# Optimization experiments

Measured on AMD Instinct MI355X. Metric: run time of the kernel, lower is better.

## Reference

```python
import jax, jax.numpy as jnp
import numpy as np

D_MODEL = 1024
N_HEAD = 16
D_HEAD = D_MODEL // N_HEAD
EXP = 4
B, T = 2, 2048
EPS = 1e-5

def setup_inputs() -> dict:
    key = jax.random.key(0)
    ks = jax.random.split(key, 16)
    s = 0.02
    return {
        "x": jax.random.normal(ks[0], (B, T, D_MODEL), jnp.float32),
        "ln1_w": jnp.ones((D_MODEL,), jnp.float32),
        "ln1_b": jnp.zeros((D_MODEL,), jnp.float32),
        "attn_w": jax.random.normal(ks[1], (D_MODEL, 3 * D_MODEL), jnp.float32) * s,
        "attn_b": jnp.zeros((3 * D_MODEL,), jnp.float32),
        "proj_w": jax.random.normal(ks[2], (D_MODEL, D_MODEL), jnp.float32) * s,
        "proj_b": jnp.zeros((D_MODEL,), jnp.float32),
        "ln2_w": jnp.ones((D_MODEL,), jnp.float32),
        "ln2_b": jnp.zeros((D_MODEL,), jnp.float32),
        "fc_w": jax.random.normal(ks[3], (D_MODEL, EXP * D_MODEL), jnp.float32) * s,
        "fc_b": jnp.zeros((EXP * D_MODEL,), jnp.float32),
        "fc2_w": jax.random.normal(ks[4], (EXP * D_MODEL, D_MODEL), jnp.float32) * s,
        "fc2_b": jnp.zeros((D_MODEL,), jnp.float32),
    }

def _layernorm(x, w, b):
    mu = jnp.mean(x, axis=-1, keepdims=True)
    var = jnp.mean(jnp.square(x - mu), axis=-1, keepdims=True)
    return (x - mu) * jax.lax.rsqrt(var + EPS) * w + b

def _attn(x, attn_w, attn_b, proj_w, proj_b):
    Bx, Tx, C = x.shape
    qkv = x @ attn_w + attn_b  # [B,T,3C]
    q, k, v = jnp.split(qkv, 3, axis=-1)
    # [B, H, T, Dh]
    q = q.reshape(Bx, Tx, N_HEAD, D_HEAD).transpose(0, 2, 1, 3)
    k = k.reshape(Bx, Tx, N_HEAD, D_HEAD).transpose(0, 2, 1, 3)
    v = v.reshape(Bx, Tx, N_HEAD, D_HEAD).transpose(0, 2, 1, 3)
    att = jnp.einsum('bhqd,bhkd->bhqk', q, k) * (1.0 / np.sqrt(D_HEAD))
    causal = jnp.tril(jnp.ones((Tx, Tx), bool))
    att = jnp.where(causal, att, -jnp.inf)
    att = jax.nn.softmax(att, axis=-1)
    y = jnp.einsum('bhqk,bhkd->bhqd', att, v)
    y = y.transpose(0, 2, 1, 3).reshape(Bx, Tx, C)
    return y @ proj_w + proj_b

def reference(x, ln1_w, ln1_b, attn_w, attn_b, proj_w, proj_b,
              ln2_w, ln2_b, fc_w, fc_b, fc2_w, fc2_b):
    x = x + _attn(_layernorm(x, ln1_w, ln1_b), attn_w, attn_b, proj_w, proj_b)
    h = _layernorm(x, ln2_w, ln2_b)
    h = jax.nn.gelu(h @ fc_w + fc_b, approximate=False)  # exact GELU (torch nn.GELU default)
    x = x + (h @ fc2_w + fc2_b)
    return x
```

## Files before the change

kernel.cpp:

```cpp
#include <hip/hip_runtime.h>
#include <hip/hip_bf16.h>
#include <math.h>


#define D_MODEL 1024
#define N_HEAD  16
#define D_HEAD  64
#define SEQ_T   2048
#define BATCH   2
#define NROWS   (BATCH * SEQ_T)
#define C3      (3 * D_MODEL)
#define D_FF    (4 * D_MODEL)

typedef __bf16 bf16x8 __attribute__((ext_vector_type(8)));
typedef __bf16 bf16x4t __attribute__((ext_vector_type(4)));
typedef short  s16x4  __attribute__((ext_vector_type(4)));
typedef float  f32x4  __attribute__((ext_vector_type(4)));

#define WAIT_VM0() asm volatile("s_waitcnt vmcnt(0)" ::: "memory")
#define WAIT_VM2() asm volatile("s_waitcnt vmcnt(2)" ::: "memory")
#define WAIT_VM4() asm volatile("s_waitcnt vmcnt(4)" ::: "memory")

__device__ __forceinline__ f32x4 mfma16_bf16(s16x4 a, s16x4 b, f32x4 c)
{
#if __has_builtin(__builtin_amdgcn_mfma_f32_16x16x16_bf16)
    return __builtin_amdgcn_mfma_f32_16x16x16_bf16(
        __builtin_bit_cast(bf16x4t, a), __builtin_bit_cast(bf16x4t, b), c, 0, 0, 0);
#else
    return __builtin_amdgcn_mfma_f32_16x16x16bf16_1k(a, b, c, 0, 0, 0);
#endif
}

__global__ __launch_bounds__(256) void ln_kernel(
    const float* __restrict__ in, const float* __restrict__ w,
    const float* __restrict__ b, __hip_bfloat16* __restrict__ out, int D)
{
    const int row = blockIdx.x;
    const int tid = threadIdx.x;
    const float* x = in + (size_t)row * 1024;

    const float4 v = *(const float4*)(x + tid * 4);
    float s  = v.x + v.y + v.z + v.w;
    float s2 = v.x * v.x + v.y * v.y + v.z * v.z + v.w * v.w;

    __shared__ float rs[256], rs2[256];
    rs[tid] = s; rs2[tid] = s2;
    __syncthreads();
    for (int off = 128; off > 0; off >>= 1) {
        if (tid < off) { rs[tid] += rs[tid + off]; rs2[tid] += rs2[tid + off]; }
        __syncthreads();
    }
    const float mu   = rs[0] * (1.0f / 1024.0f);
    const float var  = rs2[0] * (1.0f / 1024.0f) - mu * mu;
    const float rstd = rsqrtf(var + 1e-5f);

    const float4 w4 = *(const float4*)(w + tid * 4);
    const float4 b4 = *(const float4*)(b + tid * 4);
    float o[4] = {(v.x - mu) * rstd * w4.x + b4.x,
                  (v.y - mu) * rstd * w4.y + b4.y,
                  (v.z - mu) * rstd * w4.z + b4.z,
                  (v.w - mu) * rstd * w4.w + b4.w};
    ushort4 pk;
    { __hip_bfloat16 e0 = __float2bfloat16(o[0]); pk.x = *(unsigned short*)&e0;
      __hip_bfloat16 e1 = __float2bfloat16(o[1]); pk.y = *(unsigned short*)&e1;
      __hip_bfloat16 e2 = __float2bfloat16(o[2]); pk.z = *(unsigned short*)&e2;
      __hip_bfloat16 e3 = __float2bfloat16(o[3]); pk.w = *(unsigned short*)&e3; }
    *(ushort4*)(out + (size_t)row * 1024 + tid * 4) = pk;
}

__global__ __launch_bounds__(256) void prep_kernel(
    const float* __restrict__ attn_w, const float* __restrict__ proj_w,
    const float* __restrict__ fc_w,   const float* __restrict__ fc2_w,
    __hip_bfloat16* __restrict__ attn_wt, __hip_bfloat16* __restrict__ proj_wt,
    __hip_bfloat16* __restrict__ fc_wt,   __hip_bfloat16* __restrict__ fc2_wt,
    const float* __restrict__ x, const float* __restrict__ ln1_w,
    const float* __restrict__ ln1_b, __hip_bfloat16* __restrict__ ln_out)
{
    __shared__ float smem[32 * 33];
    int tb = blockIdx.x;
    const int tid = threadIdx.x;

    if (tb >= 12288) {
        const int row = tb - 12288;
        const float* xr = x + (size_t)row * 1024;
        const float4 v = *(const float4*)(xr + tid * 4);
        float s  = v.x + v.y + v.z + v.w;
        float s2 = v.x * v.x + v.y * v.y + v.z * v.z + v.w * v.w;
        float* rs  = smem;
        float* rs2 = smem + 256;
        rs[tid] = s; rs2[tid] = s2;
        __syncthreads();
        for (int off = 128; off > 0; off >>= 1) {
            if (tid < off) { rs[tid] += rs[tid + off]; rs2[tid] += rs2[tid + off]; }
            __syncthreads();
        }
        const float mu   = rs[0] * (1.0f / 1024.0f);
        const float var  = rs2[0] * (1.0f / 1024.0f) - mu * mu;
        const float rstd = rsqrtf(var + 1e-5f);
        const float4 w4 = *(const float4*)(ln1_w + tid * 4);
        const float4 b4 = *(const float4*)(ln1_b + tid * 4);
        float o[4] = {(v.x - mu) * rstd * w4.x + b4.x,
                      (v.y - mu) * rstd * w4.y + b4.y,
                      (v.z - mu) * rstd * w4.z + b4.z,
                      (v.w - mu) * rstd * w4.w + b4.w};
        ushort4 pk;
        { __hip_bfloat16 e0 = __float2bfloat16(o[0]); pk.x = *(unsigned short*)&e0;
          __hip_bfloat16 e1 = __float2bfloat16(o[1]); pk.y = *(unsigned short*)&e1;
          __hip_bfloat16 e2 = __float2bfloat16(o[2]); pk.z = *(unsigned short*)&e2;
          __hip_bfloat16 e3 = __float2bfloat16(o[3]); pk.w = *(unsigned short*)&e3; }
        *(ushort4*)(ln_out + (size_t)row * 1024 + tid * 4) = pk;
        return;
    }

    float (*t)[33] = (float(*)[33])smem;
    const float* W; __hip_bfloat16* Wt; int K, N;
    if (tb < 3072)      { W = attn_w; Wt = attn_wt; K = D_MODEL; N = C3; }
    else if (tb < 4096) { tb -= 3072; W = proj_w; Wt = proj_wt; K = D_MODEL; N = D_MODEL; }
    else if (tb < 8192) { tb -= 4096; W = fc_w;   Wt = fc_wt;   K = D_MODEL; N = D_FF; }
    else                { tb -= 8192; W = fc2_w;  Wt = fc2_wt;  K = D_FF;    N = D_MODEL; }
    const int ntx = N >> 5;
    const int k0 = (tb / ntx) * 32;
    const int n0 = (tb % ntx) * 32;

    const int row = tid >> 3;
    const int c4  = (tid & 7) * 4;

    const float4 v = *(const float4*)&W[(size_t)(k0 + row) * N + n0 + c4];
    t[row][c4 + 0] = v.x; t[row][c4 + 1] = v.y;
    t[row][c4 + 2] = v.z; t[row][c4 + 3] = v.w;
    __syncthreads();

    ushort4 pk;
    { __hip_bfloat16 e0 = __float2bfloat16(t[c4 + 0][row]); pk.x = *(unsigned short*)&e0;
      __hip_bfloat16 e1 = __float2bfloat16(t[c4 + 1][row]); pk.y = *(unsigned short*)&e1;
      __hip_bfloat16 e2 = __float2bfloat16(t[c4 + 2][row]); pk.z = *(unsigned short*)&e2;
      __hip_bfloat16 e3 = __float2bfloat16(t[c4 + 3][row]); pk.w = *(unsigned short*)&e3; }
    *(ushort4*)&Wt[(size_t)(n0 + row) * K + k0 + c4] = pk;
}

__device__ __forceinline__ void async16(const __hip_bfloat16* g, __hip_bfloat16* l)
{
    __builtin_amdgcn_global_load_lds(
        (const __attribute__((address_space(1))) void*)g,
        (__attribute__((address_space(3))) void*)l, 16, 0, 0);
}

__device__ __forceinline__ float gelu_fast(float v)
{
    const float t = v * (0.7978845608f + 0.0356774081f * v * v);
    return v / (1.0f + exp2f(-2.885390082f * t));
}

__device__ __forceinline__ void swz_xcd(int& bx, int& by)
{
    const int nbx = gridDim.x;
    const int nwg = nbx * gridDim.y;
    int lin = blockIdx.y * nbx + blockIdx.x;
    const int per = nwg >> 3;
    lin = (lin & 7) * per + (lin >> 3);
    bx = lin % nbx;
    by = lin / nbx;
}


__device__ __forceinline__ void gemm8p_core(
    const __hip_bfloat16* __restrict__ A,
    const __hip_bfloat16* __restrict__ Bt,
    int K, int row0, int col0, f32x4 (&acc)[8][4],
    __hip_bfloat16 (*Asl)[4][64 * 64], __hip_bfloat16 (*Bsl)[2][128 * 64])
{
    const int tid  = threadIdx.x;
    const int wv   = tid >> 6;
    const int lane = tid & 63;
    const int ln15 = lane & 15;
    const int lq   = lane >> 4;
    const int wr   = wv >> 2;
    const int wc   = wv & 3;

    const int srow = tid >> 3;
    const int sg   = ((tid & 7) ^ ((tid >> 3) & 7)) * 8;
    const __hip_bfloat16* Ab = A  + (size_t)(row0 + srow) * K + sg;
    const __hip_bfloat16* Bb = Bt + (size_t)(col0 + srow) * K + sg;
    const int nt = K >> 6;

#pragma unroll
    for (int mi = 0; mi < 8; ++mi)
#pragma unroll
        for (int ni = 0; ni < 4; ++ni) acc[mi][ni] = (f32x4){0.f, 0.f, 0.f, 0.f};

    auto stA = [&](int t, int buf, int b) {
        async16(Ab + (size_t)(b * 64) * K + t * 64, &Asl[buf][b][0] + tid * 8);
    };
    auto stB = [&](int t, int buf, int h) {
        async16(Bb + (size_t)(h * 128) * K + t * 64, &Bsl[buf][h][0] + tid * 8);
        async16(Bb + (size_t)(h * 128 + 64) * K + t * 64,
                &Bsl[buf][h][0] + 4096 + tid * 8);
    };

    const int rg0 = (lq ^ (ln15 & 7)) * 8;
    const int rg1 = ((4 | lq) ^ (ln15 & 7)) * 8;
    auto ldA = [&](int buf, int mi, int kk) -> bf16x8 {
        return *(const bf16x8*)&Asl[buf][wr * 2 + (mi >> 2)]
            [((mi & 3) * 16 + ln15) * 64 + (kk ? rg1 : rg0)];
    };
    auto ldB = [&](int buf, int ni, int kk) -> bf16x8 {
        return *(const bf16x8*)&Bsl[buf][wc >> 1]
            [((wc & 1) * 64 + ni * 16 + ln15) * 64 + (kk ? rg1 : rg0)];
    };

    stB(0, 0, 0); stB(0, 0, 1);
    stA(0, 0, 0); stA(0, 0, 2); stA(0, 0, 1); stA(0, 0, 3);
    WAIT_VM0();
    __builtin_amdgcn_s_barrier();

    for (int t = 0; t < nt; ++t) {
        const int pp = t & 1, op = pp ^ 1;
        const int tc = (t + 1 < nt) ? t + 1 : nt - 1;
        bf16x8 af[2][2], bfr[4][2];

#pragma unroll
        for (int m = 0; m < 2; ++m) { af[m][0] = ldA(pp, m, 0); af[m][1] = ldA(pp, m, 1); }
#pragma unroll
        for (int ni = 0; ni < 4; ++ni) { bfr[ni][0] = ldB(pp, ni, 0); bfr[ni][1] = ldB(pp, ni, 1); }
        stB(tc, op, 0);
        __builtin_amdgcn_s_barrier();
        __builtin_amdgcn_s_setprio(1);
#pragma unroll
        for (int kk = 0; kk < 2; ++kk)
#pragma unroll
            for (int m = 0; m < 2; ++m)
#pragma unroll
                for (int ni = 0; ni < 4; ++ni)
                    acc[m][ni] = __builtin_amdgcn_mfma_f32_16x16x32_bf16(
                        af[m][kk], bfr[ni][kk], acc[m][ni], 0, 0, 0);
        __builtin_amdgcn_s_setprio(0);
        __builtin_amdgcn_s_barrier();

#pragma unroll
        for (int m = 0; m < 2; ++m) { af[m][0] = ldA(pp, 2 + m, 0); af[m][1] = ldA(pp, 2 + m, 1); }
        stB(tc, op, 1);
        WAIT_VM4();
        __builtin_amdgcn_s_barrier();
        __builtin_amdgcn_s_setprio(1);
#pragma unroll
        for (int kk = 0; kk < 2; ++kk)
#pragma unroll
            for (int m = 0; m < 2; ++m)
#pragma unroll
                for (int ni = 0; ni < 4; ++ni)
                    acc[2 + m][ni] = __builtin_amdgcn_mfma_f32_16x16x32_bf16(
                        af[m][kk], bfr[ni][kk], acc[2 + m][ni], 0, 0, 0);
        __builtin_amdgcn_s_setprio(0);
        __builtin_amdgcn_s_barrier();

#pragma unroll
        for (int m = 0; m < 2; ++m) { af[m][0] = ldA(pp, 4 + m, 0); af[m][1] = ldA(pp, 4 + m, 1); }
        stA(tc, op, 0); stA(tc, op, 2);
        __builtin_amdgcn_s_barrier();
        __builtin_amdgcn_s_setprio(1);
#pragma unroll
        for (int kk = 0; kk < 2; ++kk)
#pragma unroll
            for (int m = 0; m < 2; ++m)
#pragma unroll
                for (int ni = 0; ni < 4; ++ni)
                    acc[4 + m][ni] = __builtin_amdgcn_mfma_f32_16x16x32_bf16(
                        af[m][kk], bfr[ni][kk], acc[4 + m][ni], 0, 0, 0);
        __builtin_amdgcn_s_setprio(0);
        __builtin_amdgcn_s_barrier();

#pragma unroll
        for (int m = 0; m < 2; ++m) { af[m][0] = ldA(pp, 6 + m, 0); af[m][1] = ldA(pp, 6 + m, 1); }
        stA(tc, op, 1); stA(tc, op, 3);
        WAIT_VM2();
        __builtin_amdgcn_s_barrier();
        __builtin_amdgcn_s_setprio(1);
#pragma unroll
        for (int kk = 0; kk < 2; ++kk)
#pragma unroll
            for (int m = 0; m < 2; ++m)
#pragma unroll
                for (int ni = 0; ni < 4; ++ni)
                    acc[6 + m][ni] = __builtin_amdgcn_mfma_f32_16x16x32_bf16(
                        af[m][kk], bfr[ni][kk], acc[6 + m][ni], 0, 0, 0);
        __builtin_amdgcn_s_setprio(0);
        __builtin_amdgcn_s_barrier();
    }
}

__global__ __launch_bounds__(512, 1) void gemm8p_kernel(
    const __hip_bfloat16* __restrict__ A,
    const __hip_bfloat16* __restrict__ Bt,
    const float* __restrict__ bias,
    __hip_bfloat16* __restrict__ Cout,
    int M, int N, int K, int act)
{
    __shared__ __align__(16) __hip_bfloat16 Asl[2][4][64 * 64];
    __shared__ __align__(16) __hip_bfloat16 Bsl[2][2][128 * 64];

    int bx, by;
    swz_xcd(bx, by);
    const int row0 = by * 256;
    const int col0 = bx * 256;

    f32x4 acc[8][4];
    gemm8p_core(A, Bt, K, row0, col0, acc, Asl, Bsl);

    const int tid  = threadIdx.x;
    const int wv   = tid >> 6;
    const int lane = tid & 63;
    const int ln15 = lane & 15;
    const int lq   = lane >> 4;
    const int mbase = (wv >> 2) * 128;
    const int nbase = (wv & 3) * 64;

#pragma unroll
    for (int mi = 0; mi < 8; ++mi) {
#pragma unroll
        for (int ni = 0; ni < 4; ++ni) {
            const int gc = col0 + nbase + ni * 16 + ln15;
            const float bv = bias[gc];
#pragma unroll
            for (int r = 0; r < 4; ++r) {
                const int gr = row0 + mbase + mi * 16 + lq * 4 + r;
                float v = acc[mi][ni][r] + bv;
                if (act == 1) v = gelu_fast(v);
                Cout[(size_t)gr * N + gc] = __float2bfloat16(v);
            }
        }
    }
}

__global__ __launch_bounds__(512, 1) void qkv8p_kernel(
    const __hip_bfloat16* __restrict__ A,
    const __hip_bfloat16* __restrict__ Bt,
    const float* __restrict__ bias,
    __hip_bfloat16* __restrict__ Qb,
    __hip_bfloat16* __restrict__ Kb,
    __hip_bfloat16* __restrict__ Vtb)
{
    __shared__ __align__(16) __hip_bfloat16 Asl[2][4][64 * 64];
    __shared__ __align__(16) __hip_bfloat16 Bsl[2][2][128 * 64];

    int bx, by;
    swz_xcd(bx, by);
    const int row0 = by * 256;
    const int col0 = bx * 256;

    f32x4 acc[8][4];
    gemm8p_core(A, Bt, D_MODEL, row0, col0, acc, Asl, Bsl);

    const int tid  = threadIdx.x;
    const int wv   = tid >> 6;
    const int lane = tid & 63;
    const int ln15 = lane & 15;
    const int lq   = lane >> 4;
    const int mbase = (wv >> 2) * 128;
    const int nbase = (wv & 3) * 64;

#pragma unroll
    for (int mi = 0; mi < 8; ++mi) {
        const int gr0 = row0 + mbase + mi * 16 + lq * 4;
        const int bb  = gr0 >> 11;
        const int q0  = gr0 & 2047;
#pragma unroll
        for (int ni = 0; ni < 4; ++ni) {
            const int gc  = col0 + nbase + ni * 16 + ln15;
            const float bv = bias[gc];
            const int sec = gc >> 10;
            const int hd  = (gc & 1023) >> 6;
            const int d   = gc & 63;
            if (sec == 2) {
                unsigned short u[4];
#pragma unroll
                for (int r = 0; r < 4; ++r) {
                    __hip_bfloat16 e = __float2bfloat16(acc[mi][ni][r] + bv);
                    u[r] = *(unsigned short*)&e;
                }
                uint2 pk;
                pk.x = (unsigned int)u[0] | ((unsigned int)u[1] << 16);
                pk.y = (unsigned int)u[2] | ((unsigned int)u[3] << 16);
                *(uint2*)(Vtb + ((size_t)((bb * N_HEAD + hd) * D_HEAD + d)) * SEQ_T + q0) = pk;
            } else {
                __hip_bfloat16* dst = (sec == 0 ? Qb : Kb)
                    + ((size_t)((bb * N_HEAD + hd) * SEQ_T + q0)) * D_HEAD + d;
#pragma unroll
                for (int r = 0; r < 4; ++r)
                    dst[(size_t)r * D_HEAD] = __float2bfloat16(acc[mi][ni][r] + bv);
            }
        }
    }
}

__device__ __forceinline__ void stage_db2w(
    const __hip_bfloat16* __restrict__ Ab, const __hip_bfloat16* __restrict__ Bb,
    int K, int kt, __hip_bfloat16* __restrict__ as,
    __hip_bfloat16* __restrict__ bs, int tid)
{
    const int k0 = kt * 64;
#pragma unroll
    for (int s = 0; s < 2; ++s) {
        async16(Ab + k0 + s * 32, as + s * 64 * 32 + tid * 8);
#pragma unroll
        for (int i = 0; i < 2; ++i)
            async16(Bb + (size_t)(i * 64) * K + k0 + s * 32,
                    bs + s * 128 * 32 + i * 64 * 32 + tid * 8);
    }
}

__device__ __forceinline__ void gemm_db2w(
    const __hip_bfloat16* __restrict__ A,
    const __hip_bfloat16* __restrict__ Bt,
    int K, int row0, int col0, f32x4 (&acc)[2][4])
{
    __shared__ __align__(16) __hip_bfloat16 Asl[2][2 * 64 * 32];
    __shared__ __align__(16) __hip_bfloat16 Bsl[2][2 * 128 * 32];

    const int tid  = threadIdx.x;
    const int wv   = tid >> 6;
    const int lane = tid & 63;
    const int ln15 = lane & 15;
    const int lq   = lane >> 4;
    const int mbase = (wv >> 1) * 32;
    const int nbase = (wv & 1) * 64;
    const int rcol = (lq ^ ((ln15 >> 1) & 3)) * 8;
    const int ssw  = ((tid & 3) ^ ((tid >> 3) & 3)) * 8;
    const __hip_bfloat16* Ab = A  + (size_t)(row0 + (tid >> 2)) * K + ssw;
    const __hip_bfloat16* Bb = Bt + (size_t)(col0 + (tid >> 2)) * K + ssw;
    const int nt = K >> 6;

#pragma unroll
    for (int mi = 0; mi < 2; ++mi)
#pragma unroll
        for (int ni = 0; ni < 4; ++ni) acc[mi][ni] = (f32x4){0.f, 0.f, 0.f, 0.f};

    stage_db2w(Ab, Bb, K, 0, &Asl[0][0], &Bsl[0][0], tid);
    WAIT_VM0();
    __builtin_amdgcn_s_barrier();

    for (int t = 0; t < nt; ++t) {
        const int p   = t & 1;
        const int tcl = (t + 1 < nt) ? t + 1 : nt - 1;
        bf16x8 af[2][2], bfr[2][4];

#pragma unroll
        for (int s = 0; s < 2; ++s) {
#pragma unroll
            for (int mi = 0; mi < 2; ++mi)
                af[s][mi] = *(const bf16x8*)
                    &Asl[p][s * 64 * 32 + (mbase + mi * 16 + ln15) * 32 + rcol];
#pragma unroll
            for (int ni = 0; ni < 4; ++ni)
                bfr[s][ni] = *(const bf16x8*)
                    &Bsl[p][s * 128 * 32 + (nbase + ni * 16 + ln15) * 32 + rcol];
        }

        stage_db2w(Ab, Bb, K, tcl, &Asl[p ^ 1][0], &Bsl[p ^ 1][0], tid);

        __builtin_amdgcn_s_setprio(1);
#pragma unroll
        for (int s = 0; s < 2; ++s)
#pragma unroll
            for (int mi = 0; mi < 2; ++mi)
#pragma unroll
                for (int ni = 0; ni < 4; ++ni)
                    acc[mi][ni] = __builtin_amdgcn_mfma_f32_16x16x32_bf16(
                        af[s][mi], bfr[s][ni], acc[mi][ni], 0, 0, 0);
        __builtin_amdgcn_s_setprio(0);

        WAIT_VM0();
        __builtin_amdgcn_s_barrier();
    }
}

__global__ __launch_bounds__(256, 3) void gemm64_kernel(
    const __hip_bfloat16* __restrict__ A,
    const __hip_bfloat16* __restrict__ Bt,
    const float* __restrict__ bias,
    const float* __restrict__ residual,
    void* __restrict__ Cout,
    int M, int N, int K, int act, int outBf16)
{
    int bx, by;
    swz_xcd(bx, by);
    const int row0 = by * 64;
    const int col0 = bx * 128;

    f32x4 acc[2][4];
    gemm_db2w(A, Bt, K, row0, col0, acc);

    const int tid  = threadIdx.x;
    const int wv   = tid >> 6;
    const int lane = tid & 63;
    const int ln15 = lane & 15;
    const int lq   = lane >> 4;
    const int mbase = (wv >> 1) * 32;
    const int nbase = (wv & 1) * 64;

#pragma unroll
    for (int mi = 0; mi < 2; ++mi) {
#pragma unroll
        for (int ni = 0; ni < 4; ++ni) {
            const int gc = col0 + nbase + ni * 16 + ln15;
            const float bv = bias[gc];
#pragma unroll
            for (int r = 0; r < 4; ++r) {
                const int gr = row0 + mbase + mi * 16 + lq * 4 + r;
                float v = acc[mi][ni][r] + bv;
                if (act == 1) v = gelu_fast(v);
                if (residual) v += residual[(size_t)gr * N + gc];
                if (outBf16)
                    ((__hip_bfloat16*)Cout)[(size_t)gr * N + gc] = __float2bfloat16(v);
                else
                    ((float*)Cout)[(size_t)gr * N + gc] = v;
            }
        }
    }
}

#define ATQ 64
#define ATK 128
#define NQT (SEQ_T / ATQ)
#define VP2 136

__global__ __launch_bounds__(256) void mfma_attn_kernel(
    const __hip_bfloat16* __restrict__ Qb,
    const __hip_bfloat16* __restrict__ Kb,
    const __hip_bfloat16* __restrict__ Vtb,
    __hip_bfloat16* __restrict__ y)
{
    __shared__ __align__(16) __hip_bfloat16 Ks[2 * ATK * 32];
    __shared__ __align__(16) __hip_bfloat16 Vts[D_HEAD * VP2];

    const int flat = (blockIdx.z * gridDim.y + blockIdx.y) * gridDim.x + blockIdx.x;
    const int xcd  = flat & 7;
    const int slot = flat >> 3;
    const int pair = slot & 15;
    const int hb   = slot >> 4;
    const int h    = xcd + 8 * (hb & 1);
    const int b    = hb >> 1;

    const int tid  = threadIdx.x;
    const int wv   = tid >> 6;
    const int lane = tid & 63;
    const int ln15 = lane & 15;
    const int lq   = lane >> 4;

    const __hip_bfloat16* Qh = Qb  + (size_t)(b * N_HEAD + h) * SEQ_T * D_HEAD;
    const __hip_bfloat16* Kh = Kb  + (size_t)(b * N_HEAD + h) * SEQ_T * D_HEAD;
    const __hip_bfloat16* Vh = Vtb + (size_t)(b * N_HEAD + h) * D_HEAD * SEQ_T;
    const size_t bT = (size_t)b * SEQ_T;

    const float CEXP = 0.18033688011f;
    const float DTHR = 8.0f / CEXP;

    bf16x8 kreg[4], vreg[4];
    const int kr = tid >> 3, kg = tid & 7;
    const int vr = tid >> 4, vc = tid & 15;
    const int khalf = kg >> 2;
    const int kpos  = (kg & 3) ^ ((kr >> 1) & 3);

    auto issue = [&](int kb) {
#pragma unroll
        for (int i = 0; i < 4; ++i)
            kreg[i] = *(const bf16x8*)(Kh + (size_t)(kb + kr + i * 32) * D_HEAD + kg * 8);
#pragma unroll
        for (int i = 0; i < 4; ++i)
            vreg[i] = *(const bf16x8*)(Vh + (size_t)(vr + i * 16) * SEQ_T + kb + vc * 8);
    };
    auto commit = [&]() {
#pragma unroll
        for (int i = 0; i < 4; ++i) {
            const int r = kr + i * 32;
            *(bf16x8*)&Ks[khalf * (ATK * 32) + r * 32 + kpos * 8] = kreg[i];
        }
#pragma unroll
        for (int i = 0; i < 4; ++i) {
            const int r = vr + i * 16;
            *(bf16x8*)&Vts[r * VP2 + vc * 8] = vreg[i];
        }
    };

    const int rcol = (lq ^ ((ln15 >> 1) & 3)) * 8;

#pragma unroll 1
    for (int half = 0; half < 2; ++half) {
        const int qt    = half == 0 ? pair : (NQT - 1 - pair);
        const int qbase = qt * ATQ;
        const int ntk   = (qt >> 1) + 1;
        const int qg    = qbase + wv * 16 + ln15;

        bf16x8 qf[2];
#pragma unroll
        for (int kc = 0; kc < 2; ++kc)
            qf[kc] = *(const bf16x8*)(Qh + (size_t)(qbase + wv * 16 + ln15) * D_HEAD
                                      + kc * 32 + lq * 8);

        f32x4 Oacc[4];
#pragma unroll
        for (int dn = 0; dn < 4; ++dn) Oacc[dn] = (f32x4){0.f, 0.f, 0.f, 0.f};
        float m_run = -INFINITY, l_run = 0.f;

        issue(0);

        for (int t = 0; t < ntk; ++t) {
            const int kb = t * ATK;
            commit();
            __syncthreads();
            if (t + 1 < ntk) issue((t + 1) * ATK);

            f32x4 st[8];
#pragma unroll
            for (int jf = 0; jf < 8; ++jf) st[jf] = (f32x4){0.f, 0.f, 0.f, 0.f};
            __builtin_amdgcn_s_setprio(1);
#pragma unroll
            for (int jf = 0; jf < 8; ++jf) {
                const int rw = jf * 16 + ln15;
                const bf16x8 kf0 = *(const bf16x8*)&Ks[rw * 32 + rcol];
                const bf16x8 kf1 = *(const bf16x8*)&Ks[ATK * 32 + rw * 32 + rcol];
                st[jf] = __builtin_amdgcn_mfma_f32_16x16x32_bf16(kf0, qf[0], st[jf], 0, 0, 0);
                st[jf] = __builtin_amdgcn_mfma_f32_16x16x32_bf16(kf1, qf[1], st[jf], 0, 0, 0);
            }
            __builtin_amdgcn_s_setprio(0);

            if (t == ntk - 1) {
#pragma unroll
                for (int jf = 0; jf < 8; ++jf)
#pragma unroll
                    for (int r = 0; r < 4; ++r)
                        if ((kb + jf * 16 + lq * 4 + r) > qg) st[jf][r] = -INFINITY;
            }

            float tmax = st[0][0];
#pragma unroll
            for (int jf = 0; jf < 8; ++jf)
#pragma unroll
                for (int r = 0; r < 4; ++r) tmax = fmaxf(tmax, st[jf][r]);
            tmax = fmaxf(tmax, __shfl_xor(tmax, 16));
            tmax = fmaxf(tmax, __shfl_xor(tmax, 32));

            if (!__all(tmax <= m_run + DTHR)) {
                const float mnew  = fmaxf(m_run, tmax);
                const float alpha = exp2f((m_run - mnew) * CEXP);
                l_run *= alpha;
                m_run = mnew;
                float a4[4];
#pragma unroll
                for (int r = 0; r < 4; ++r) a4[r] = __shfl(alpha, lq * 4 + r);
#pragma unroll
                for (int dn = 0; dn < 4; ++dn)
#pragma unroll
                    for (int r = 0; r < 4; ++r) Oacc[dn][r] *= a4[r];
            }
            const float mc = m_run * CEXP;
            float psum = 0.f;
#pragma unroll
            for (int jf = 0; jf < 8; ++jf)
#pragma unroll
                for (int r = 0; r < 4; ++r) {
                    const float p = exp2f(fmaf(st[jf][r], CEXP, -mc));
                    st[jf][r] = p;
                    psum += p;
                }
            psum += __shfl_xor(psum, 16);
            psum += __shfl_xor(psum, 32);
            l_run += psum;

            __builtin_amdgcn_s_setprio(1);
#pragma unroll
            for (int jf = 0; jf < 8; ++jf) {
                s16x4 pfr;
#pragma unroll
                for (int s = 0; s < 4; ++s) {
                    __hip_bfloat16 e = __float2bfloat16(st[jf][s]);
                    pfr[s] = __builtin_bit_cast(short, e);
                }
#pragma unroll
                for (int dn = 0; dn < 4; ++dn) {
                    const s16x4 vfr = *(const s16x4*)&Vts[(dn * 16 + ln15) * VP2
                                                          + jf * 16 + lq * 4];
                    Oacc[dn] = mfma16_bf16(pfr, vfr, Oacc[dn]);
                }
            }
            __builtin_amdgcn_s_setprio(0);
            __syncthreads();
        }

        float il[4];
#pragma unroll
        for (int r = 0; r < 4; ++r) il[r] = 1.0f / __shfl(l_run, lq * 4 + r);
#pragma unroll
        for (int dn = 0; dn < 4; ++dn)
#pragma unroll
            for (int r = 0; r < 4; ++r)
                Ks[(wv * 16 + lq * 4 + r) * 72 + dn * 16 + ln15] =
                    __float2bfloat16(Oacc[dn][r] * il[r]);
        const int r2 = lane >> 3, c8 = (lane & 7) * 8;
#pragma unroll
        for (int i = 0; i < 2; ++i) {
            const int row = wv * 16 + r2 + 8 * i;
            const bf16x8 val = *(const bf16x8*)&Ks[row * 72 + c8];
            *(bf16x8*)(y + (bT + qbase + row) * D_MODEL + h * D_HEAD + c8) = val;
        }
        __syncthreads();
    }
}

extern "C" void kernel_launch(void* const* d_in, const int* in_sizes, int n_in,
                              void* d_out, int out_size, void* d_ws, size_t ws_size,
                              hipStream_t stream)
{
    const float* x      = (const float*)d_in[0];
    const float* ln1_w  = (const float*)d_in[1];
    const float* ln1_b  = (const float*)d_in[2];
    const float* attn_w = (const float*)d_in[3];
    const float* attn_b = (const float*)d_in[4];
    const float* proj_w = (const float*)d_in[5];
    const float* proj_b = (const float*)d_in[6];
    const float* ln2_w  = (const float*)d_in[7];
    const float* ln2_b  = (const float*)d_in[8];
    const float* fc_w   = (const float*)d_in[9];
    const float* fc_b   = (const float*)d_in[10];
    const float* fc2_w  = (const float*)d_in[11];
    const float* fc2_b  = (const float*)d_in[12];
    float* out = (float*)d_out;

    char* ws = (char*)d_ws;
    __hip_bfloat16* Qb      = (__hip_bfloat16*)(ws);
    __hip_bfloat16* Kb      = (__hip_bfloat16*)(ws + (size_t)8  * 1024 * 1024);
    __hip_bfloat16* Vtb     = (__hip_bfloat16*)(ws + (size_t)16 * 1024 * 1024);
    __hip_bfloat16* h_bf    = (__hip_bfloat16*)(ws);
    __hip_bfloat16* ln_buf  = (__hip_bfloat16*)(ws + (size_t)32 * 1024 * 1024);
    __hip_bfloat16* y_buf   = (__hip_bfloat16*)(ws + (size_t)40 * 1024 * 1024);
    float*          xmid    = (float*)(ws + (size_t)48 * 1024 * 1024);
    __hip_bfloat16* attn_wt = (__hip_bfloat16*)(ws + (size_t)64 * 1024 * 1024);
    __hip_bfloat16* proj_wt = (__hip_bfloat16*)(ws + (size_t)70 * 1024 * 1024);
    __hip_bfloat16* fc_wt   = (__hip_bfloat16*)(ws + (size_t)72 * 1024 * 1024);
    __hip_bfloat16* fc2_wt  = (__hip_bfloat16*)(ws + (size_t)80 * 1024 * 1024);

    dim3 blk256(256);
    dim3 blk512(512);

    prep_kernel<<<dim3(12288 + NROWS), blk256, 0, stream>>>(
        attn_w, proj_w, fc_w, fc2_w, attn_wt, proj_wt, fc_wt, fc2_wt,
        x, ln1_w, ln1_b, ln_buf);

    qkv8p_kernel<<<dim3(C3 / 256, NROWS / 256), blk512, 0, stream>>>(
        ln_buf, attn_wt, attn_b, Qb, Kb, Vtb);

    mfma_attn_kernel<<<dim3(NQT / 2, N_HEAD, BATCH), blk256, 0, stream>>>(
        Qb, Kb, Vtb, y_buf);

    gemm64_kernel<<<dim3(D_MODEL / 128, NROWS / 64), blk256, 0, stream>>>(
        y_buf, proj_wt, proj_b, x, xmid, NROWS, D_MODEL, D_MODEL, 0, 0);

    ln_kernel<<<dim3(NROWS), blk256, 0, stream>>>(xmid, ln2_w, ln2_b, ln_buf, D_MODEL);

    gemm8p_kernel<<<dim3(D_FF / 256, NROWS / 256), blk512, 0, stream>>>(
        ln_buf, fc_wt, fc_b, h_bf, NROWS, D_FF, D_MODEL, 1);

    gemm64_kernel<<<dim3(D_MODEL / 128, NROWS / 64), blk256, 0, stream>>>(
        h_bf, fc2_wt, fc2_b, xmid, out, NROWS, D_MODEL, D_FF, 0, 0);
}
```

Before: 340.8 us.

## Double-buffer attention K/V tiles in LDS with async K loads

The attention kernel now keeps two LDS buffers for the K and V tiles. K is loaded straight from global memory into LDS through async16 with an XOR swizzle over a full 64-wide row. V is still staged through registers but written into the alternating buffer. This lets the per-iteration trailing barrier go away and removes the register round-trip for K, so the next tile's load overlaps with the current tile's compute. The cost is roughly doubled LDS use per block, which may reduce how many blocks fit on a compute unit.

```diff
diff --git a/kernel.cpp b/kernel.cpp
--- a/kernel.cpp
+++ b/kernel.cpp
@@ -529,8 +529,8 @@
     const __hip_bfloat16* __restrict__ Vtb,
     __hip_bfloat16* __restrict__ y)
 {
-    __shared__ __align__(16) __hip_bfloat16 Ks[2 * ATK * 32];
-    __shared__ __align__(16) __hip_bfloat16 Vts[D_HEAD * VP2];
+    __shared__ __align__(16) __hip_bfloat16 Ks[2][ATK * 64];
+    __shared__ __align__(16) __hip_bfloat16 Vts[2][D_HEAD * VP2];
 
     const int flat = (blockIdx.z * gridDim.y + blockIdx.y) * gridDim.x + blockIdx.x;
     const int xcd  = flat & 7;
@@ -554,34 +554,30 @@
     const float CEXP = 0.18033688011f;
     const float DTHR = 8.0f / CEXP;
 
-    bf16x8 kreg[4], vreg[4];
-    const int kr = tid >> 3, kg = tid & 7;
+    const int kr  = tid >> 3, kg = tid & 7;
+    const int ksg = (kg ^ (kr & 7)) * 8;
+    bf16x8 vreg[4];
     const int vr = tid >> 4, vc = tid & 15;
-    const int khalf = kg >> 2;
-    const int kpos  = (kg & 3) ^ ((kr >> 1) & 3);
-
-    auto issue = [&](int kb) {
+
+    auto issueK = [&](int kb, int buf) {
 #pragma unroll
         for (int i = 0; i < 4; ++i)
-            kreg[i] = *(const bf16x8*)(Kh + (size_t)(kb + kr + i * 32) * D_HEAD + kg * 8);
+            async16(Kh + (size_t)(kb + kr + i * 32) * D_HEAD + ksg,
+                    &Ks[buf][i * 2048] + tid * 8);
+    };
+    auto issueV = [&](int kb) {
 #pragma unroll
         for (int i = 0; i < 4; ++i)
             vreg[i] = *(const bf16x8*)(Vh + (size_t)(vr + i * 16) * SEQ_T + kb + vc * 8);
     };
-    auto commit = [&]() {
-#pragma unroll
-        for (int i = 0; i < 4; ++i) {
-            const int r = kr + i * 32;
-            *(bf16x8*)&Ks[khalf * (ATK * 32) + r * 32 + kpos * 8] = kreg[i];
-        }
-#pragma unroll
-        for (int i = 0; i < 4; ++i) {
-            const int r = vr + i * 16;
-            *(bf16x8*)&Vts[r * VP2 + vc * 8] = vreg[i];
-        }
+    auto commitV = [&](int buf) {
+#pragma unroll
+        for (int i = 0; i < 4; ++i)
+            *(bf16x8*)&Vts[buf][(vr + i * 16) * VP2 + vc * 8] = vreg[i];
     };
 
-    const int rcol = (lq ^ ((ln15 >> 1) & 3)) * 8;
+    const int rg0 = (lq ^ (ln15 & 7)) * 8;
+    const int rg1 = ((4 | lq) ^ (ln15 & 7)) * 8;
 
 #pragma unroll 1
     for (int half = 0; half < 2; ++half) {
@@ -601,13 +597,18 @@
         for (int dn = 0; dn < 4; ++dn) Oacc[dn] = (f32x4){0.f, 0.f, 0.f, 0.f};
         float m_run = -INFINITY, l_run = 0.f;
 
-        issue(0);
+        issueK(0, 0);
+        issueV(0);
 
         for (int t = 0; t < ntk; ++t) {
-            const int kb = t * ATK;
-            commit();
+            const int kb  = t * ATK;
+            const int buf = t & 1;
+            commitV(buf);
             __syncthreads();
-            if (t + 1 < ntk) issue((t + 1) * ATK);
+            if (t + 1 < ntk) {
+                issueK((t + 1) * ATK, buf ^ 1);
+                issueV((t + 1) * ATK);
+            }
 
             f32x4 st[8];
 #pragma unroll
@@ -616,8 +617,8 @@
 #pragma unroll
             for (int jf = 0; jf < 8; ++jf) {
                 const int rw = jf * 16 + ln15;
-                const bf16x8 kf0 = *(const bf16x8*)&Ks[rw * 32 + rcol];
-                const bf16x8 kf1 = *(const bf16x8*)&Ks[ATK * 32 + rw * 32 + rcol];
+                const bf16x8 kf0 = *(const bf16x8*)&Ks[buf][rw * 64 + rg0];
+                const bf16x8 kf1 = *(const bf16x8*)&Ks[buf][rw * 64 + rg1];
                 st[jf] = __builtin_amdgcn_mfma_f32_16x16x32_bf16(kf0, qf[0], st[jf], 0, 0, 0);
                 st[jf] = __builtin_amdgcn_mfma_f32_16x16x32_bf16(kf1, qf[1], st[jf], 0, 0, 0);
             }
@@ -677,15 +678,15 @@
                 }
 #pragma unroll
                 for (int dn = 0; dn < 4; ++dn) {
-                    const s16x4 vfr = *(const s16x4*)&Vts[(dn * 16 + ln15) * VP2
-                                                          + jf * 16 + lq * 4];
+                    const s16x4 vfr = *(const s16x4*)&Vts[buf][(dn * 16 + ln15) * VP2
+                                                            + jf * 16 + lq * 4];
                     Oacc[dn] = mfma16_bf16(pfr, vfr, Oacc[dn]);
                 }
             }
             __builtin_amdgcn_s_setprio(0);
-            __syncthreads();
         }
 
+        __syncthreads();
         float il[4];
 #pragma unroll
         for (int r = 0; r < 4; ++r) il[r] = 1.0f / __shfl(l_run, lq * 4 + r);
@@ -693,13 +694,14 @@
         for (int dn = 0; dn < 4; ++dn)
 #pragma unroll
             for (int r = 0; r < 4; ++r)
-                Ks[(wv * 16 + lq * 4 + r) * 72 + dn * 16 + ln15] =
+                Ks[0][(wv * 16 + lq * 4 + r) * 72 + dn * 16 + ln15] =
                     __float2bfloat16(Oacc[dn][r] * il[r]);
+        __syncthreads();
         const int r2 = lane >> 3, c8 = (lane & 7) * 8;
 #pragma unroll
         for (int i = 0; i < 2; ++i) {
             const int row = wv * 16 + r2 + 8 * i;
-            const bf16x8 val = *(const bf16x8*)&Ks[row * 72 + c8];
+            const bf16x8 val = *(const bf16x8*)&Ks[0][row * 72 + c8];
             *(bf16x8*)(y + (bT + qbase + row) * D_MODEL + h * D_HEAD + c8) = val;
         }
         __syncthreads();
```

Result: no change. 340.3 us (-0.1%).
